# Optimization experiments

Hardware: AMD Instinct MI355X
Metric: run time of the kernel (lower is better)

## Reference

```python
import jax, jax.numpy as jnp
import numpy as np

N = 100000   # nodes
E = 1600000  # directed edges
F_IN, F_HID, F_OUT = 10, 64, 4


def setup_inputs() -> dict:
    key = jax.random.key(0)
    ks = jax.random.split(key, 8)
    x = jax.random.normal(ks[0], (N, F_IN), dtype=jnp.float32)
    edge_index = jax.random.randint(ks[1], (2, E), 0, N, dtype=jnp.int64)
    W1 = jax.random.normal(ks[2], (F_IN, F_HID), dtype=jnp.float32) * (1.0 / np.sqrt(F_IN))
    b1 = jnp.zeros((F_HID,), dtype=jnp.float32)
    W2 = jax.random.normal(ks[3], (F_HID, F_HID), dtype=jnp.float32) * (1.0 / np.sqrt(F_HID))
    b2 = jnp.zeros((F_HID,), dtype=jnp.float32)
    W3 = jax.random.normal(ks[4], (F_HID, F_OUT), dtype=jnp.float32) * (1.0 / np.sqrt(F_HID))
    b3 = jnp.zeros((F_OUT,), dtype=jnp.float32)
    return {"x": x, "edge_index": edge_index, "W1": W1, "b1": b1,
            "W2": W2, "b2": b2, "W3": W3, "b3": b3}


def _gcn_layer(h_in, W, b, src, dst, dinv_sqrt):
    # GCNConv: D^{-1/2} (A + I) D^{-1/2} (h_in W) + b, with deg counted incl. self-loops
    h = h_in @ W                                   # [N, F_out]
    norm = dinv_sqrt[src] * dinv_sqrt[dst]         # [E]
    msg = h[src] * norm[:, None]                   # [E, F_out]  (dominant traffic)
    agg = jax.ops.segment_sum(msg, dst, num_segments=N)
    agg = agg + h * (dinv_sqrt * dinv_sqrt)[:, None]  # self-loop contribution
    return agg + b


def reference(x, edge_index, W1, b1, W2, b2, W3, b3):
    src, dst = edge_index[0], edge_index[1]
    # degree of target nodes including self-loop
    deg = jax.ops.segment_sum(jnp.ones((E,), x.dtype), dst, num_segments=N) + 1.0
    dinv_sqrt = jax.lax.rsqrt(deg)
    h = jax.nn.relu(_gcn_layer(x, W1, b1, src, dst, dinv_sqrt))
    # dropout is identity in eval mode (training=False)
    h = jax.nn.relu(_gcn_layer(h, W2, b2, src, dst, dinv_sqrt))
    h = _gcn_layer(h, W3, b3, src, dst, dinv_sqrt)
    return jax.nn.log_softmax(h, axis=1)
```

## Files before the change

kernel.cpp:

```cpp
#include <hip/hip_runtime.h>
#include <hip/hip_bf16.h>
#include <math.h>


#define D_MAX 48
#define BUCK_SH 8
#define NPB 256
#define NBK 391
#define P1_BLOCKS 256
#define P1_THREADS 512
#define SEG_CAP 32
#define OFL_CAP 8192

typedef __hip_bfloat16 bf16;
typedef int int4v __attribute__((ext_vector_type(4)));
typedef unsigned short ushort8v __attribute__((ext_vector_type(8)));

__global__ void k_bin(const int* __restrict__ src, const int* __restrict__ dst,
                      int* __restrict__ arena, int* __restrict__ cnt2,
                      int* __restrict__ ofl_cnt, int2* __restrict__ ofl, int E) {
    __shared__ int stage[NBK][SEG_CAP];
    __shared__ int lcnt[NBK];
    int t = threadIdx.x, blk = blockIdx.x;
    for (int i = t; i < NBK; i += P1_THREADS) lcnt[i] = 0;
    __syncthreads();
#define BIN_ONE(d_, s_) {                                                   \
        int b_ = (d_) >> BUCK_SH;                                           \
        int rec_ = ((d_) & (NPB - 1)) | ((s_) << BUCK_SH);                  \
        int slot_ = atomicAdd(&lcnt[b_], 1);                                \
        if (slot_ < SEG_CAP) stage[b_][slot_] = rec_;                       \
        else {                                                              \
            int p_ = atomicAdd(ofl_cnt, 1);                                 \
            if (p_ < OFL_CAP) ofl[p_] = make_int2(b_, rec_);                \
        }                                                                   \
    }
    int E4 = E >> 2;
    int chunk4 = (E4 + P1_BLOCKS - 1) / P1_BLOCKS;
    int q0 = blk * chunk4;
    int q1 = min(q0 + chunk4, E4);
    for (int q = q0 + t; q < q1; q += P1_THREADS) {
        int4v d4 = __builtin_nontemporal_load((const int4v*)dst + q);
        int4v s4 = __builtin_nontemporal_load((const int4v*)src + q);
        BIN_ONE(d4.x, s4.x);
        BIN_ONE(d4.y, s4.y);
        BIN_ONE(d4.z, s4.z);
        BIN_ONE(d4.w, s4.w);
    }
    if (blk == 0 && t < (E & 3)) {
        int e = (E & ~3) + t;
        BIN_ONE(dst[e], src[e]);
    }
#undef BIN_ONE
    __syncthreads();
    for (int b = t; b < NBK; b += P1_THREADS)
        cnt2[b * P1_BLOCKS + blk] = lcnt[b];
    for (int i = t; i < NBK * 8; i += P1_THREADS) {
        int b = i >> 3, q = i & 7;
        int cc = min(lcnt[b], SEG_CAP);
        if (q * 4 < cc) {
            int4v v = ((const int4v*)&stage[b][0])[q];
            ((int4v*)arena)[((size_t)b * P1_BLOCKS + blk) * (SEG_CAP / 4) + q] = v;
        }
    }
}

__global__ void k_ellbuild(const int* __restrict__ arena, const int* __restrict__ cnt2,
                           const int* __restrict__ ofl_cnt, const int2* __restrict__ ofl,
                           const float* __restrict__ x,
                           int* __restrict__ ell, int* __restrict__ cnt,
                           float* __restrict__ dinv, bf16* __restrict__ xp, int N) {
    __shared__ int ellb[NPB * D_MAX];
    __shared__ int cntL[NPB];
    __shared__ float dloc[NPB];
    int t = threadIdx.x, b = blockIdx.x;
    cntL[t] = 0;
    __syncthreads();
#define INS_ONE(rec_) {                                                     \
        int r_ = (rec_) & (NPB - 1);                                        \
        int s_ = (rec_) >> BUCK_SH;                                         \
        int slot_ = atomicAdd(&cntL[r_], 1);                                \
        if (slot_ < D_MAX) ellb[r_ * D_MAX + slot_] = s_;                   \
    }
    int cc = min(cnt2[b * P1_BLOCKS + t], SEG_CAP);
    const int4v* segv = (const int4v*)(arena + ((size_t)b * P1_BLOCKS + t) * SEG_CAP);
    for (int i4 = 0; i4 * 4 < cc; ++i4) {
        int4v r4 = segv[i4];
        int lim = cc - i4 * 4;
        INS_ONE(r4.x);
        if (lim > 1) INS_ONE(r4.y);
        if (lim > 2) INS_ONE(r4.z);
        if (lim > 3) INS_ONE(r4.w);
    }
    int total = min(*ofl_cnt, OFL_CAP);
    for (int i = t; i < total; i += NPB) {
        int2 r = ofl[i];
        if (r.x == b) INS_ONE(r.y);
    }
#undef INS_ONE
    __syncthreads();
    int nb = b << BUCK_SH;
    int n = nb + t;
    if (n < N) {
        int dg = cntL[t];
        cnt[n] = dg;
        float dv = rsqrtf((float)dg + 1.0f);
        dinv[n] = dv;
        dloc[t] = dv;
    }
    __syncthreads();
    const int ROWQ = D_MAX / 4;
    for (int i4 = t; i4 < NPB * ROWQ; i4 += NPB) {
        int nn = nb + i4 / ROWQ;
        if (nn < N)
            ((int4v*)(ell + (size_t)nb * D_MAX))[i4] = ((const int4v*)ellb)[i4];
    }
    for (int i = t; i < NPB * 10; i += NPB) {
        int nn = nb + i / 10;
        if (nn < N) xp[(size_t)nb * 10 + i] = __float2bfloat16(x[(size_t)nb * 10 + i] * dloc[i / 10]);
    }
}

__global__ void k_gather10(const int* __restrict__ ell, const int* __restrict__ cnt,
                           const bf16* __restrict__ xp, const float* __restrict__ dinv,
                           float* __restrict__ aggx, int N) {
    int tid = threadIdx.x;
    int g = tid & 15;
    int node = blockIdx.x * 16 + (tid >> 4);
    if (node >= N) return;
    int deg = cnt[node]; if (deg > D_MAX) deg = D_MAX;
    float acc = 0.0f;
    for (int c0 = 0; c0 < deg; c0 += 16) {
        int m = deg - c0; if (m > 16) m = 16;
        int sid = 0;
        if (g < m) sid = ell[(size_t)node * D_MAX + c0 + g];
        for (int i = 0; i < m; ++i) {
            int s = __shfl(sid, i, 16);
            if (g < 10) acc += __bfloat162float(xp[(size_t)s * 10 + g]);
        }
    }
    if (g < 10) {
        acc += __bfloat162float(xp[(size_t)node * 10 + g]);
        aggx[(size_t)node * 10 + g] = dinv[node] * acc;
    }
}

__global__ void k_fused1(const float* __restrict__ aggx, const float* __restrict__ W1,
                         const float* __restrict__ b1, const float* __restrict__ W2,
                         const float* __restrict__ dinv, bf16* __restrict__ t, int N) {
    __shared__ float W1s[10 * 64];
    __shared__ unsigned short h1b[64][64];
    int tid = threadIdx.x;
    int f = tid & 63, w = tid >> 6;
    float w2c[64];
#pragma unroll
    for (int k = 0; k < 64; ++k) w2c[k] = W2[k * 64 + f];
    for (int i = tid; i < 640; i += 256) W1s[i] = W1[i];
    __syncthreads();
    int nb = blockIdx.x * 64;
    float bf = b1[f];
    for (int j = 0; j < 16; ++j) {
        int ln = w * 16 + j;
        int n = nb + ln;
        float acc = bf;
        if (n < N) {
#pragma unroll
            for (int k = 0; k < 10; ++k)
                acc = fmaf(aggx[(size_t)n * 10 + k], W1s[k * 64 + f], acc);
        }
        h1b[ln][f] = __bfloat16_as_ushort(__float2bfloat16(fmaxf(acc, 0.0f)));
    }
    __syncthreads();
    for (int j = 0; j < 16; ++j) {
        int ln = w * 16 + j;
        int n = nb + ln;
        if (n >= N) continue;
        float acc = 0.0f;
        const ushort8v* hr = (const ushort8v*)&h1b[ln][0];
#pragma unroll
        for (int k8 = 0; k8 < 8; ++k8) {
            ushort8v h8 = hr[k8];
#pragma unroll
            for (int jj = 0; jj < 8; ++jj) {
                float hv = __uint_as_float(((unsigned)h8[jj]) << 16);
                acc = fmaf(hv, w2c[k8 * 8 + jj], acc);
            }
        }
        t[(size_t)n * 64 + f] = __float2bfloat16(acc * dinv[n]);
    }
}

__global__ void k_fused2(const int* __restrict__ ell, const int* __restrict__ cnt,
                         const bf16* __restrict__ t, const float* __restrict__ dinv,
                         const float* __restrict__ b2, const float* __restrict__ W3,
                         float* __restrict__ t3, int N) {
    __shared__ float W3s[256];
    int tid = threadIdx.x;
    W3s[tid] = W3[tid];
    __syncthreads();
    int f = tid & 63;
    int node = blockIdx.x * 4 + (tid >> 6);
    if (node >= N) return;
    int deg = cnt[node]; if (deg > D_MAX) deg = D_MAX;
    int sid = 0;
    if (f < deg) sid = ell[(size_t)node * D_MAX + f];
    float acc = 0.0f;
    int i = 0;
    for (; i + 8 <= deg; i += 8) {
        int s0 = __shfl(sid, i),     s1 = __shfl(sid, i + 1);
        int s2 = __shfl(sid, i + 2), s3 = __shfl(sid, i + 3);
        int s4 = __shfl(sid, i + 4), s5 = __shfl(sid, i + 5);
        int s6 = __shfl(sid, i + 6), s7 = __shfl(sid, i + 7);
        float v0 = __bfloat162float(t[(size_t)s0 * 64 + f]);
        float v1 = __bfloat162float(t[(size_t)s1 * 64 + f]);
        float v2 = __bfloat162float(t[(size_t)s2 * 64 + f]);
        float v3 = __bfloat162float(t[(size_t)s3 * 64 + f]);
        float v4 = __bfloat162float(t[(size_t)s4 * 64 + f]);
        float v5 = __bfloat162float(t[(size_t)s5 * 64 + f]);
        float v6 = __bfloat162float(t[(size_t)s6 * 64 + f]);
        float v7 = __bfloat162float(t[(size_t)s7 * 64 + f]);
        acc += ((v0 + v1) + (v2 + v3)) + ((v4 + v5) + (v6 + v7));
    }
    for (; i < deg; ++i) {
        int s = __shfl(sid, i);
        acc += __bfloat162float(t[(size_t)s * 64 + f]);
    }
    float di = dinv[node];
    acc += __bfloat162float(t[(size_t)node * 64 + f]);
    float h2 = fmaxf(di * acc + b2[f], 0.0f);
    float p0 = h2 * W3s[f * 4 + 0];
    float p1 = h2 * W3s[f * 4 + 1];
    float p2 = h2 * W3s[f * 4 + 2];
    float p3 = h2 * W3s[f * 4 + 3];
#pragma unroll
    for (int off = 32; off > 0; off >>= 1) {
        p0 += __shfl_down(p0, off);
        p1 += __shfl_down(p1, off);
        p2 += __shfl_down(p2, off);
        p3 += __shfl_down(p3, off);
    }
    if (f == 0) {
        float4 r = {p0 * di, p1 * di, p2 * di, p3 * di};
        *(float4*)(t3 + (size_t)node * 4) = r;
    }
}

__global__ void k_out(const int* __restrict__ ell, const int* __restrict__ cnt,
                      const float* __restrict__ t3, const float* __restrict__ dinv,
                      const float* __restrict__ b3, float* __restrict__ out, int N) {
    int n = blockIdx.x * blockDim.x + threadIdx.x;
    if (n >= N) return;
    int deg = cnt[n]; if (deg > D_MAX) deg = D_MAX;
    float a0 = 0.f, a1 = 0.f, a2 = 0.f, a3 = 0.f;
    const int* row = ell + (size_t)n * D_MAX;
    for (int c = 0; c < deg; c += 4) {
        int4 q = *(const int4*)(row + c);
        {
            float4 v = *(const float4*)(t3 + (size_t)q.x * 4);
            a0 += v.x; a1 += v.y; a2 += v.z; a3 += v.w;
        }
        if (c + 1 < deg) {
            float4 v = *(const float4*)(t3 + (size_t)q.y * 4);
            a0 += v.x; a1 += v.y; a2 += v.z; a3 += v.w;
        }
        if (c + 2 < deg) {
            float4 v = *(const float4*)(t3 + (size_t)q.z * 4);
            a0 += v.x; a1 += v.y; a2 += v.z; a3 += v.w;
        }
        if (c + 3 < deg) {
            float4 v = *(const float4*)(t3 + (size_t)q.w * 4);
            a0 += v.x; a1 += v.y; a2 += v.z; a3 += v.w;
        }
    }
    float4 sv = *(const float4*)(t3 + (size_t)n * 4);
    a0 += sv.x; a1 += sv.y; a2 += sv.z; a3 += sv.w;
    float di = dinv[n];
    float v0 = di * a0 + b3[0];
    float v1 = di * a1 + b3[1];
    float v2 = di * a2 + b3[2];
    float v3 = di * a3 + b3[3];
    float m = fmaxf(fmaxf(v0, v1), fmaxf(v2, v3));
    float s = expf(v0 - m) + expf(v1 - m) + expf(v2 - m) + expf(v3 - m);
    float ls = m + logf(s);
    float4 r = {v0 - ls, v1 - ls, v2 - ls, v3 - ls};
    *(float4*)(out + (size_t)n * 4) = r;
}

extern "C" void kernel_launch(void* const* d_in, const int* in_sizes, int n_in,
                              void* d_out, int out_size, void* d_ws, size_t ws_size,
                              hipStream_t stream) {
    const float* x  = (const float*)d_in[0];
    const int*   ei = (const int*)d_in[1];
    const float* W1 = (const float*)d_in[2];
    const float* b1 = (const float*)d_in[3];
    const float* W2 = (const float*)d_in[4];
    const float* b2 = (const float*)d_in[5];
    const float* W3 = (const float*)d_in[6];
    const float* b3 = (const float*)d_in[7];
    float* out = (float*)d_out;

    const int E = in_sizes[1] / 2;
    const int N = in_sizes[0] / 10;
    const int* src = ei;
    const int* dst = ei + E;

    float* dinv    = (float*)d_ws;
    int*   cnt     = (int*)(dinv + N);
    int*   ell     = cnt + N;
    bf16*  xp      = (bf16*)(ell + (size_t)N * D_MAX);
    float* t3      = (float*)(xp + (size_t)N * 10 + 8);
    int*   ofl_cnt = (int*)(t3 + (size_t)N * 4);
    int2*  ofl     = (int2*)(ofl_cnt + 4);
    int*   arena   = (int*)(ofl + OFL_CAP);
    int*   cnt2    = arena + (size_t)NBK * P1_BLOCKS * SEG_CAP;
    float* aggx    = (float*)arena;
    bf16*  tbuf    = (bf16*)(aggx + (size_t)N * 10);

    hipMemsetAsync(ofl_cnt, 0, 4 * sizeof(int), stream);
    k_bin<<<P1_BLOCKS, P1_THREADS, 0, stream>>>(src, dst, arena, cnt2, ofl_cnt, ofl, E);
    k_ellbuild<<<NBK, NPB, 0, stream>>>(arena, cnt2, ofl_cnt, ofl, x, ell, cnt, dinv, xp, N);

    k_gather10<<<(N + 15) / 16, 256, 0, stream>>>(ell, cnt, xp, dinv, aggx, N);
    k_fused1<<<(N + 63) / 64, 256, 0, stream>>>(aggx, W1, b1, W2, dinv, tbuf, N);
    k_fused2<<<(N + 3) / 4, 256, 0, stream>>>(ell, cnt, tbuf, dinv, b2, W3, t3, N);
    k_out<<<(N + 255) / 256, 256, 0, stream>>>(ell, cnt, t3, dinv, b3, out, N);
}
```

Measured before the change: 173.7 us.

## Retune binning grid, pad xp rows to 16, split FMA chains, widen fused2 blocks

This bundles several unrelated tweaks. It doubles the binning grid while halving the per-segment cap, and the ELL builder now reads two segments per thread. It pads the bf16 scaled-feature rows from 10 to 16 so the gather loads are aligned and unpredicated. It splits the dependent FMA chains in fused1 into two accumulators for more instruction-level parallelism, and launches fused2 with 512-thread blocks covering 8 nodes each. The smaller segment cap may push more edges into the overflow path, which every ELL-build block scans, and the padded rows add gather traffic.

```diff
diff --git a/kernel.cpp b/kernel.cpp
--- a/kernel.cpp
+++ b/kernel.cpp
@@ -7,10 +7,11 @@
 #define BUCK_SH 8
 #define NPB 256
 #define NBK 391
-#define P1_BLOCKS 256
+#define P1_BLOCKS 512
 #define P1_THREADS 512
-#define SEG_CAP 32
-#define OFL_CAP 8192
+#define SEG_CAP 16
+#define OFL_CAP 16384
+#define XPW 16
 
 typedef __hip_bfloat16 bf16;
 typedef int int4v __attribute__((ext_vector_type(4)));
@@ -54,8 +55,8 @@
     __syncthreads();
     for (int b = t; b < NBK; b += P1_THREADS)
         cnt2[b * P1_BLOCKS + blk] = lcnt[b];
-    for (int i = t; i < NBK * 8; i += P1_THREADS) {
-        int b = i >> 3, q = i & 7;
+    for (int i = t; i < NBK * (SEG_CAP / 4); i += P1_THREADS) {
+        int b = i >> 2, q = i & 3;
         int cc = min(lcnt[b], SEG_CAP);
         if (q * 4 < cc) {
             int4v v = ((const int4v*)&stage[b][0])[q];
@@ -81,15 +82,18 @@
         int slot_ = atomicAdd(&cntL[r_], 1);                                \
         if (slot_ < D_MAX) ellb[r_ * D_MAX + slot_] = s_;                   \
     }
-    int cc = min(cnt2[b * P1_BLOCKS + t], SEG_CAP);
-    const int4v* segv = (const int4v*)(arena + ((size_t)b * P1_BLOCKS + t) * SEG_CAP);
-    for (int i4 = 0; i4 * 4 < cc; ++i4) {
-        int4v r4 = segv[i4];
-        int lim = cc - i4 * 4;
-        INS_ONE(r4.x);
-        if (lim > 1) INS_ONE(r4.y);
-        if (lim > 2) INS_ONE(r4.z);
-        if (lim > 3) INS_ONE(r4.w);
+    for (int ss = 0; ss < P1_BLOCKS / NPB; ++ss) {
+        int seg = ss * NPB + t;
+        int cc = min(cnt2[b * P1_BLOCKS + seg], SEG_CAP);
+        const int4v* segv = (const int4v*)(arena + ((size_t)b * P1_BLOCKS + seg) * SEG_CAP);
+        for (int i4 = 0; i4 * 4 < cc; ++i4) {
+            int4v r4 = segv[i4];
+            int lim = cc - i4 * 4;
+            INS_ONE(r4.x);
+            if (lim > 1) INS_ONE(r4.y);
+            if (lim > 2) INS_ONE(r4.z);
+            if (lim > 3) INS_ONE(r4.w);
+        }
     }
     int total = min(*ofl_cnt, OFL_CAP);
     for (int i = t; i < total; i += NPB) {
@@ -114,9 +118,13 @@
         if (nn < N)
             ((int4v*)(ell + (size_t)nb * D_MAX))[i4] = ((const int4v*)ellb)[i4];
     }
-    for (int i = t; i < NPB * 10; i += NPB) {
-        int nn = nb + i / 10;
-        if (nn < N) xp[(size_t)nb * 10 + i] = __float2bfloat16(x[(size_t)nb * 10 + i] * dloc[i / 10]);
+    for (int i = t; i < NPB * XPW; i += NPB) {
+        int ln = i / XPW, g = i & (XPW - 1);
+        int nn = nb + ln;
+        if (nn < N) {
+            float v = (g < 10) ? x[(size_t)nn * 10 + g] * dloc[ln] : 0.0f;
+            xp[(size_t)nb * XPW + i] = __float2bfloat16(v);
+        }
     }
 }
 
@@ -135,13 +143,11 @@
         if (g < m) sid = ell[(size_t)node * D_MAX + c0 + g];
         for (int i = 0; i < m; ++i) {
             int s = __shfl(sid, i, 16);
-            if (g < 10) acc += __bfloat162float(xp[(size_t)s * 10 + g]);
-        }
-    }
-    if (g < 10) {
-        acc += __bfloat162float(xp[(size_t)node * 10 + g]);
-        aggx[(size_t)node * 10 + g] = dinv[node] * acc;
-    }
+            acc += __bfloat162float(xp[(size_t)s * XPW + g]);
+        }
+    }
+    acc += __bfloat162float(xp[(size_t)node * XPW + g]);
+    if (g < 10) aggx[(size_t)node * 10 + g] = dinv[node] * acc;
 }
 
 __global__ void k_fused1(const float* __restrict__ aggx, const float* __restrict__ W1,
@@ -161,31 +167,36 @@
     for (int j = 0; j < 16; ++j) {
         int ln = w * 16 + j;
         int n = nb + ln;
-        float acc = bf;
+        float a0 = bf, a1 = 0.0f;
         if (n < N) {
 #pragma unroll
-            for (int k = 0; k < 10; ++k)
-                acc = fmaf(aggx[(size_t)n * 10 + k], W1s[k * 64 + f], acc);
-        }
-        h1b[ln][f] = __bfloat16_as_ushort(__float2bfloat16(fmaxf(acc, 0.0f)));
+            for (int k = 0; k < 5; ++k) {
+                a0 = fmaf(aggx[(size_t)n * 10 + k], W1s[k * 64 + f], a0);
+                a1 = fmaf(aggx[(size_t)n * 10 + 5 + k], W1s[(5 + k) * 64 + f], a1);
+            }
+        }
+        h1b[ln][f] = __bfloat16_as_ushort(__float2bfloat16(fmaxf(a0 + a1, 0.0f)));
     }
     __syncthreads();
     for (int j = 0; j < 16; ++j) {
         int ln = w * 16 + j;
         int n = nb + ln;
         if (n >= N) continue;
-        float acc = 0.0f;
+        float acc0 = 0.0f, acc1 = 0.0f;
         const ushort8v* hr = (const ushort8v*)&h1b[ln][0];
 #pragma unroll
-        for (int k8 = 0; k8 < 8; ++k8) {
-            ushort8v h8 = hr[k8];
+        for (int k8 = 0; k8 < 4; ++k8) {
+            ushort8v h8a = hr[k8];
+            ushort8v h8b = hr[k8 + 4];
 #pragma unroll
             for (int jj = 0; jj < 8; ++jj) {
-                float hv = __uint_as_float(((unsigned)h8[jj]) << 16);
-                acc = fmaf(hv, w2c[k8 * 8 + jj], acc);
+                float hva = __uint_as_float(((unsigned)h8a[jj]) << 16);
+                float hvb = __uint_as_float(((unsigned)h8b[jj]) << 16);
+                acc0 = fmaf(hva, w2c[k8 * 8 + jj], acc0);
+                acc1 = fmaf(hvb, w2c[32 + k8 * 8 + jj], acc1);
             }
         }
-        t[(size_t)n * 64 + f] = __float2bfloat16(acc * dinv[n]);
+        t[(size_t)n * 64 + f] = __float2bfloat16((acc0 + acc1) * dinv[n]);
     }
 }
 
@@ -195,10 +206,10 @@
                          float* __restrict__ t3, int N) {
     __shared__ float W3s[256];
     int tid = threadIdx.x;
-    W3s[tid] = W3[tid];
+    if (tid < 256) W3s[tid] = W3[tid];
     __syncthreads();
     int f = tid & 63;
-    int node = blockIdx.x * 4 + (tid >> 6);
+    int node = blockIdx.x * 8 + (tid >> 6);
     if (node >= N) return;
     int deg = cnt[node]; if (deg > D_MAX) deg = D_MAX;
     int sid = 0;
@@ -307,7 +318,7 @@
     int*   cnt     = (int*)(dinv + N);
     int*   ell     = cnt + N;
     bf16*  xp      = (bf16*)(ell + (size_t)N * D_MAX);
-    float* t3      = (float*)(xp + (size_t)N * 10 + 8);
+    float* t3      = (float*)(xp + (size_t)N * XPW);
     int*   ofl_cnt = (int*)(t3 + (size_t)N * 4);
     int2*  ofl     = (int2*)(ofl_cnt + 4);
     int*   arena   = (int*)(ofl + OFL_CAP);
@@ -321,6 +332,6 @@
 
     k_gather10<<<(N + 15) / 16, 256, 0, stream>>>(ell, cnt, xp, dinv, aggx, N);
     k_fused1<<<(N + 63) / 64, 256, 0, stream>>>(aggx, W1, b1, W2, dinv, tbuf, N);
-    k_fused2<<<(N + 3) / 4, 256, 0, stream>>>(ell, cnt, tbuf, dinv, b2, W3, t3, N);
+    k_fused2<<<(N + 7) / 8, 512, 0, stream>>>(ell, cnt, tbuf, dinv, b2, W3, t3, N);
     k_out<<<(N + 255) / 256, 256, 0, stream>>>(ell, cnt, t3, dinv, b3, out, N);
 }
```

Result: slower. 195.8 us (+12.7%).
